# Kernel optimization log

Measured on AMD Instinct MI355X. Metric: run time of the kernel, lower is better.

## Reference

```python
import jax, jax.numpy as jnp
import numpy as np

BN_EPS = 1e-5

def setup_inputs() -> dict:
    key = jax.random.key(0)
    ks = jax.random.split(key, 4)
    B, C, H, W = 8, 64, 128, 128
    return {
        "x": jax.random.normal(ks[0], (B, C, H, W), jnp.float32),
        "w_reduce": jax.random.normal(ks[1], (C, C), jnp.float32) * 0.05,
        "b_reduce": jnp.zeros((C,), jnp.float32),
        "bn_gamma": jnp.ones((C,), jnp.float32),
        "bn_beta": jnp.zeros((C,), jnp.float32),
        "w_span": jax.random.normal(ks[2], (9, C), jnp.float32) * 0.05,
        "b_span": jnp.zeros((9,), jnp.float32),
        "w_conv2": jax.random.normal(ks[3], (C, C, 3, 3), jnp.float32) * 0.02,
        "b_conv2": jnp.zeros((C,), jnp.float32),
    }


def _involution(x, w_reduce, b_reduce, bn_gamma, bn_beta, w_span, b_span):
    # Involution2d: in_ch == out_ch so initial_mapping is Identity; groups=1, reduce_ratio=1, stride=1.
    B, C, H, W = x.shape
    # unfold 3x3, pad 1 -> patches [B, C, 9, H, W] (torch unfold ordering: C major, then kh, kw)
    xp = jnp.pad(x, ((0, 0), (0, 0), (1, 1), (1, 1)))
    patches = jnp.stack(
        [xp[:, :, i:i + H, j:j + W] for i in range(3) for j in range(3)], axis=2
    )  # [B, C, 9, H, W]
    # kernel generation: 1x1 conv -> BatchNorm2d (batch stats) -> ReLU -> 1x1 conv
    r = jnp.einsum('oc,bchw->bohw', w_reduce, x) + b_reduce[None, :, None, None]
    mu = r.mean(axis=(0, 2, 3), keepdims=True)
    var = r.var(axis=(0, 2, 3), keepdims=True)
    rn = (r - mu) * jax.lax.rsqrt(var + BN_EPS)
    rn = jax.nn.relu(rn * bn_gamma[None, :, None, None] + bn_beta[None, :, None, None])
    kern = jnp.einsum('kc,bchw->bkhw', w_span, rn) + b_span[None, :, None, None]  # [B, 9, H, W]
    # per-pixel dynamic kernel applied to patches, summed over kernel axis
    return jnp.einsum('bkhw,bckhw->bchw', kern, patches)


def reference(x, w_reduce, b_reduce, bn_gamma, bn_beta, w_span, b_span, w_conv2, b_conv2):
    z = jax.nn.softplus(_involution(x, w_reduce, b_reduce, bn_gamma, bn_beta, w_span, b_span))
    y = jax.lax.conv_general_dilated(z, w_conv2, window_strides=(1, 1), padding=((1, 1), (1, 1)))
    y = y + b_conv2[None, :, None, None]
    return jax.nn.softplus(y)
```

## Files before the change

kernel.cpp:

```cpp
#include <hip/hip_runtime.h>
#include <math.h>

#define H_ 128
#define W_ 128
#define C_ 64
#define B_ 8
#define HW 16384
#define NPIX (B_*HW)

typedef __attribute__((ext_vector_type(8))) short short8;
typedef __attribute__((ext_vector_type(4))) float f32x4;

__device__ __forceinline__ float softplus_fast(float v) {
    return fmaxf(v, 0.f) + __logf(1.f + __expf(-fabsf(v)));
}

__device__ __forceinline__ unsigned short f2bf(float f) {
    unsigned u = __builtin_bit_cast(unsigned, f);
    unsigned r = (u + 0x7fffu + ((u >> 16) & 1u)) >> 16;
    return (unsigned short)r;
}

__device__ __forceinline__ void gl_lds16(const float* g, float* l) {
    __builtin_amdgcn_global_load_lds(
        (const __attribute__((address_space(1))) void*)g,
        (__attribute__((address_space(3))) void*)l, 16, 0, 0);
}

__global__ __launch_bounds__(256) void k0_wtr(const float* __restrict__ w2,
                                              const float* __restrict__ wr,
                                              const float* __restrict__ wspan,
                                              unsigned short* __restrict__ wtr,
                                              unsigned short* __restrict__ wtr1,
                                              unsigned short* __restrict__ wtr2,
                                              float* __restrict__ stats)
{
    int t = blockIdx.x * 256 + threadIdx.x;
    if (t < 256) stats[t] = 0.f;
    if (t < 512) {
        int lane = t & 63, f = t >> 6;
        int mt = f >> 1, kh = f & 1;
        int o  = mt * 16 + (lane & 15);
        int c0 = kh * 32 + ((lane >> 4) << 3);
        uint4 pk;
        unsigned short* pv = (unsigned short*)&pk;
#pragma unroll
        for (int e = 0; e < 8; ++e)
            pv[e] = f2bf(wr[o * C_ + c0 + e]);
        *(uint4*)&wtr1[(size_t)t * 8] = pk;
    } else if (t < 640) {
        int tt = t - 512;
        int lane = tt & 63, kh = tt >> 6;
        int o  = lane & 15;
        int c0 = (kh << 5) + ((lane >> 4) << 3);
        uint4 pk;
        unsigned short* pv = (unsigned short*)&pk;
#pragma unroll
        for (int e = 0; e < 8; ++e)
            pv[e] = (o < 9) ? f2bf(wspan[o * C_ + c0 + e]) : (unsigned short)0;
        *(uint4*)&wtr2[(size_t)tt * 8] = pk;
    }
    if (t >= 4 * 18 * 64) return;
    int lane = t & 63;
    int f    = (t >> 6) % 18;
    int wv   = t / (18 * 64);
    int koff = f >> 1, ch = f & 1;
    int o = wv * 16 + (lane & 15);
    int cb = ch * 32 + ((lane >> 4) << 3);
    uint4 pk;
    unsigned short* pv = (unsigned short*)&pk;
#pragma unroll
    for (int e = 0; e < 8; ++e)
        pv[e] = f2bf(w2[(size_t)o * 576 + (size_t)(cb + e) * 9 + koff]);
    *(uint4*)&wtr[(size_t)t * 8] = pk;
}

__global__ __launch_bounds__(256) void k1_mfma(
    const float* __restrict__ x, const unsigned short* __restrict__ wtr1,
    const float* __restrict__ br, unsigned short* __restrict__ rb,
    float* __restrict__ stats)
{
    __shared__ unsigned short xb[256 * 64];
    __shared__ float brs[C_];
    __shared__ float ls[128];
    int tid = threadIdx.x;
    int blk = blockIdx.x;
    int pid0 = blk << 8;
    int b    = pid0 >> 14;
    int rem0 = pid0 & (HW - 1);
    const float* xbase = x + (((size_t)b * C_) << 14) + rem0;

    if (tid < C_) brs[tid] = br[tid];
    if (tid < 128) ls[tid] = 0.f;

    int p = tid;
#pragma unroll
    for (int m = 0; m < 8; ++m) {
        float tmp[8];
#pragma unroll
        for (int e = 0; e < 8; ++e)
            tmp[e] = xbase[((size_t)(m * 8 + e) << 14) + p];
        unsigned pk[4];
#pragma unroll
        for (int e = 0; e < 4; ++e)
            pk[e] = (unsigned)f2bf(tmp[2 * e]) | ((unsigned)f2bf(tmp[2 * e + 1]) << 16);
        *(uint4*)&xb[(p << 6) + ((m ^ (p & 7)) << 3)] = *(uint4*)pk;
    }

    int wid = tid >> 6, lane = tid & 63;
    int nl  = lane & 15;
    int kg  = lane >> 4;

    short8 af[8];
    const short8* wp = (const short8*)wtr1;
#pragma unroll
    for (int f = 0; f < 8; ++f) af[f] = wp[f * 64 + lane];

    f32x4 acc[4][4];
#pragma unroll
    for (int mt = 0; mt < 4; ++mt)
#pragma unroll
        for (int nt = 0; nt < 4; ++nt) acc[mt][nt] = (f32x4){0.f, 0.f, 0.f, 0.f};

    __syncthreads();

    int nbase = wid << 6;
#pragma unroll
    for (int nt = 0; nt < 4; ++nt) {
        int pp = nbase + (nt << 4) + nl;
#pragma unroll
        for (int kh = 0; kh < 2; ++kh) {
            int m = kh * 4 + kg;
            short8 bf = *(const short8*)&xb[(pp << 6) + ((m ^ (pp & 7)) << 3)];
#pragma unroll
            for (int mt = 0; mt < 4; ++mt)
                acc[mt][nt] = __builtin_amdgcn_mfma_f32_16x16x32_bf16(
                    af[mt * 2 + kh], bf, acc[mt][nt], 0, 0, 0);
        }
    }

    __syncthreads();

    float s_[16], q_[16];
#pragma unroll
    for (int i = 0; i < 16; ++i) { s_[i] = 0.f; q_[i] = 0.f; }

#pragma unroll
    for (int mt = 0; mt < 4; ++mt) {
        int c = (mt << 4) + (kg << 2);
        float b0 = brs[c], b1 = brs[c + 1], b2v = brs[c + 2], b3 = brs[c + 3];
        int chunk = c >> 3;
#pragma unroll
        for (int nt = 0; nt < 4; ++nt) {
            int pp = nbase + (nt << 4) + nl;
            f32x4 a = acc[mt][nt];
            float v0 = a[0] + b0, v1 = a[1] + b1, v2 = a[2] + b2v, v3 = a[3] + b3;
            s_[mt * 4 + 0] += v0; q_[mt * 4 + 0] += v0 * v0;
            s_[mt * 4 + 1] += v1; q_[mt * 4 + 1] += v1 * v1;
            s_[mt * 4 + 2] += v2; q_[mt * 4 + 2] += v2 * v2;
            s_[mt * 4 + 3] += v3; q_[mt * 4 + 3] += v3 * v3;
            unsigned lo = (unsigned)f2bf(v0) | ((unsigned)f2bf(v1) << 16);
            unsigned hi = (unsigned)f2bf(v2) | ((unsigned)f2bf(v3) << 16);
            unsigned* dst = (unsigned*)&xb[(pp << 6) + ((chunk ^ (pp & 7)) << 3) + ((kg & 1) << 2)];
            dst[0] = lo;
            dst[1] = hi;
        }
    }

#pragma unroll
    for (int i = 0; i < 16; ++i) {
#pragma unroll
        for (int m = 1; m <= 8; m <<= 1) {
            s_[i] += __shfl_xor(s_[i], m, 64);
            q_[i] += __shfl_xor(q_[i], m, 64);
        }
    }
    if (nl == 0) {
#pragma unroll
        for (int i = 0; i < 16; ++i) {
            int c = ((i >> 2) << 4) + (kg << 2) + (i & 3);
            atomicAdd(&ls[c], s_[i]);
            atomicAdd(&ls[64 + c], q_[i]);
        }
    }
    __syncthreads();
    if (tid < 128) atomicAdd(&stats[tid], ls[tid]);

    uint4* rp = (uint4*)(rb + ((size_t)(pid0 + p) << 6));
#pragma unroll
    for (int m = 0; m < 8; ++m)
        rp[m] = *(const uint4*)&xb[(p << 6) + ((m ^ (p & 7)) << 3)];
}

__global__ __launch_bounds__(256) void k34_fused(
    const float* __restrict__ x, const unsigned short* __restrict__ rb,
    const float* __restrict__ stats, const float* __restrict__ gamma,
    const float* __restrict__ beta, const unsigned short* __restrict__ wtr2,
    const float* __restrict__ bspan, const unsigned short* __restrict__ wtr,
    const float* __restrict__ b2, float* __restrict__ out)
{
    __shared__ float xh0[8 * 20 * 24], xh1[8 * 20 * 24];
    __shared__ unsigned short zt[324 * 64];
    __shared__ float a_s[C_], c_s[C_];

    int tid = threadIdx.x;
    if (tid < C_) {
        float inv_n = 1.f / (float)NPIX;
        float mu  = stats[tid] * inv_n;
        float var = stats[C_ + tid] * inv_n - mu * mu;
        float is  = rsqrtf(var + 1e-5f);
        float a   = gamma[tid] * is;
        a_s[tid] = a;
        c_s[tid] = beta[tid] - mu * a;
    }

    int blk = blockIdx.x;
    int b = blk >> 6, t = blk & 63;
    int h0 = (t >> 3) << 4, w0 = (t & 7) << 4;
    const float* xb_ = x + (((size_t)b * C_) << 14);
    const float* zgz = stats + 128;

    int goff[4];
#pragma unroll
    for (int k = 0; k < 4; ++k) {
        int item = (k << 8) + tid;
        int c    = item / 120;
        int rem  = item - c * 120;
        int row  = rem / 6;
        int ii   = rem - row * 6;
        int gh   = h0 + row - 2;
        int gw   = w0 - 4 + (ii << 2);
        bool ok = (item < 960) && ((unsigned)gh < 128u) && ((unsigned)gw < 128u);
        goff[k] = ok ? ((c << 14) + (gh << 7) + gw) : -1;
    }

    auto stage = [&](int g, float* buf) {
#pragma unroll
        for (int k = 0; k < 4; ++k) {
            if (k < 3 || tid < 192) {
                int item = (k << 8) + tid;
                const float* src = (goff[k] >= 0) ? (xb_ + (g << 17) + goff[k]) : zgz;
                gl_lds16(src, buf + (item << 2));
            }
        }
    };

    int lane = tid & 63;
    int w_  = tid >> 6;
    int nl  = lane & 15;
    int kg  = lane >> 4;
    short8 af0 = ((const short8*)wtr2)[lane];
    short8 af1 = ((const short8*)wtr2)[64 + lane];

    stage(0, xh0);
    __syncthreads();
    stage(1, xh1);

    float aa[2][8], cc[2][8];
#pragma unroll
    for (int kh = 0; kh < 2; ++kh) {
        int cb = (kh << 5) + (kg << 3);
#pragma unroll
        for (int e = 0; e < 8; ++e) { aa[kh][e] = a_s[cb + e]; cc[kh][e] = c_s[cb + e]; }
    }

    float* kl = (float*)zt;
#pragma unroll
    for (int nt = 0; nt < 6; ++nt) {
        int col = (nt << 2) + w_;
        if (col < 21) {
            int hp = (col << 4) + nl;
            int py = hp / 18, px = hp - py * 18;
            int gh = h0 + py - 1, gw = w0 + px - 1;
            int ghc = min(max(gh, 0), 127), gwc = min(max(gw, 0), 127);
            int pid2 = (b << 14) + (ghc << 7) + gwc;
            f32x4 acc9 = (f32x4){0.f, 0.f, 0.f, 0.f};
#pragma unroll
            for (int kh = 0; kh < 2; ++kh) {
                uint4 rv = *(const uint4*)(rb + ((size_t)pid2 << 6) + (kh << 5) + (kg << 3));
                const unsigned* ru = (const unsigned*)&rv;
                unsigned po[4];
#pragma unroll
                for (int e2 = 0; e2 < 4; ++e2) {
                    float lo = __builtin_bit_cast(float, ru[e2] << 16);
                    float hi = __builtin_bit_cast(float, ru[e2] & 0xffff0000u);
                    float r0 = fmaxf(aa[kh][2 * e2]     * lo + cc[kh][2 * e2],     0.f);
                    float r1 = fmaxf(aa[kh][2 * e2 + 1] * hi + cc[kh][2 * e2 + 1], 0.f);
                    po[e2] = (unsigned)f2bf(r0) | ((unsigned)f2bf(r1) << 16);
                }
                short8 bfrag = __builtin_bit_cast(short8, *(uint4*)po);
                acc9 = __builtin_amdgcn_mfma_f32_16x16x32_bf16(
                    kh ? af1 : af0, bfrag, acc9, 0, 0, 0);
            }
#pragma unroll
            for (int e = 0; e < 4; ++e) {
                int rr = (kg << 2) + e;
                if (rr < 9) kl[hp * 9 + rr] = acc9[e];
            }
        }
    }
    __syncthreads();

    float kern0[9], kern1[9];
#pragma unroll
    for (int k = 0; k < 9; ++k) kern0[k] = kl[tid * 9 + k] + bspan[k];
    bool has2 = tid < 68;
    if (has2) {
#pragma unroll
        for (int k = 0; k < 9; ++k) kern1[k] = kl[(256 + tid) * 9 + k] + bspan[k];
    }
    __syncthreads();

    int py0 = tid / 18, px0 = tid - py0 * 18;
    bool ib0 = ((unsigned)(h0 + py0 - 1) < 128u) && ((unsigned)(w0 + px0 - 1) < 128u);
    int hp1 = 256 + tid;
    int py1 = hp1 / 18, px1 = hp1 - py1 * 18;
    bool ib1 = has2 && ((unsigned)(h0 + py1 - 1) < 128u) && ((unsigned)(w0 + px1 - 1) < 128u);

    short8 wf[18];
    const short8* wp = (const short8*)wtr;
#pragma unroll
    for (int f = 0; f < 18; ++f)
        wf[f] = wp[(size_t)(w_ * 18 + f) * 64 + lane];

#pragma unroll 1
    for (int g = 0; g < 8; ++g) {
        if (g >= 1 && g < 7) stage(g + 1, (g & 1) ? xh0 : xh1);
        const float* xf = (g & 1) ? xh1 : xh0;

        unsigned pk[4];
        if (ib0) {
#pragma unroll
            for (int cp = 0; cp < 4; ++cp) {
                const float* p0 = xf + (cp * 2) * 480 + py0 * 24 + px0 + 2;
                const float* p1 = p0 + 480;
                float acc0 = 0.f, acc1 = 0.f;
#pragma unroll
                for (int i = 0; i < 3; ++i)
#pragma unroll
                    for (int j = 0; j < 3; ++j) {
                        float kv = kern0[i * 3 + j];
                        acc0 += kv * p0[i * 24 + j];
                        acc1 += kv * p1[i * 24 + j];
                    }
                pk[cp] = (unsigned)f2bf(softplus_fast(acc0))
                       | ((unsigned)f2bf(softplus_fast(acc1)) << 16);
            }
        } else {
#pragma unroll
            for (int cp = 0; cp < 4; ++cp) pk[cp] = 0u;
        }
        *(uint4*)&zt[(tid << 6) + ((g ^ (tid & 7)) << 3)] = *(uint4*)pk;

        if (has2) {
            if (ib1) {
#pragma unroll
                for (int cp = 0; cp < 4; ++cp) {
                    const float* p0 = xf + (cp * 2) * 480 + py1 * 24 + px1 + 2;
                    const float* p1 = p0 + 480;
                    float acc0 = 0.f, acc1 = 0.f;
#pragma unroll
                    for (int i = 0; i < 3; ++i)
#pragma unroll
                        for (int j = 0; j < 3; ++j) {
                            float kv = kern1[i * 3 + j];
                            acc0 += kv * p0[i * 24 + j];
                            acc1 += kv * p1[i * 24 + j];
                        }
                    pk[cp] = (unsigned)f2bf(softplus_fast(acc0))
                           | ((unsigned)f2bf(softplus_fast(acc1)) << 16);
                }
            } else {
#pragma unroll
                for (int cp = 0; cp < 4; ++cp) pk[cp] = 0u;
            }
            *(uint4*)&zt[(hp1 << 6) + ((g ^ (hp1 & 7)) << 3)] = *(uint4*)pk;
        }
        if (g < 7) __syncthreads();
    }
    __syncthreads();

    f32x4 acc[16];
#pragma unroll
    for (int nt = 0; nt < 16; ++nt) acc[nt] = (f32x4){0.f, 0.f, 0.f, 0.f};

#pragma unroll
    for (int y = 0; y < 18; ++y) {
        short8 bf[6];
#pragma unroll
        for (int j = 0; j < 3; ++j)
#pragma unroll
            for (int ch = 0; ch < 2; ++ch) {
                int p  = y * 18 + j + nl;
                int cg = ch * 4 + kg;
                bf[j * 2 + ch] = *(const short8*)&zt[(p << 6) + ((cg ^ (p & 7)) << 3)];
            }
#pragma unroll
        for (int i = 0; i < 3; ++i) {
            int nt = y - i;
            if (nt >= 0 && nt < 16) {
#pragma unroll
                for (int j = 0; j < 3; ++j)
#pragma unroll
                    for (int ch = 0; ch < 2; ++ch)
                        acc[nt] = __builtin_amdgcn_mfma_f32_16x16x32_bf16(
                            wf[(i * 3 + j) * 2 + ch], bf[j * 2 + ch], acc[nt], 0, 0, 0);
            }
        }
    }

    float bias[4];
#pragma unroll
    for (int r = 0; r < 4; ++r) bias[r] = b2[(w_ << 4) + (kg << 2) + r];

    size_t ob = ((size_t)b) << 20;
#pragma unroll
    for (int nt = 0; nt < 16; ++nt) {
        int h = h0 + nt;
#pragma unroll
        for (int r = 0; r < 4; ++r) {
            int o = (w_ << 4) + (kg << 2) + r;
            float v = acc[nt][r] + bias[r];
            out[ob + ((size_t)o << 14) + (h << 7) + w0 + nl] = softplus_fast(v);
        }
    }
}

extern "C" void kernel_launch(void* const* d_in, const int* in_sizes, int n_in,
                              void* d_out, int out_size, void* d_ws, size_t ws_size,
                              hipStream_t stream)
{
    const float* x   = (const float*)d_in[0];
    const float* wr  = (const float*)d_in[1];
    const float* br  = (const float*)d_in[2];
    const float* gam = (const float*)d_in[3];
    const float* bet = (const float*)d_in[4];
    const float* wsp = (const float*)d_in[5];
    const float* bsp = (const float*)d_in[6];
    const float* w2  = (const float*)d_in[7];
    const float* b2  = (const float*)d_in[8];
    float* out = (float*)d_out;

    unsigned short* rb   = (unsigned short*)d_ws;
    unsigned short* wtr  = rb + (size_t)NPIX * C_;
    unsigned short* wtr1 = wtr + 4608 * 8;
    unsigned short* wtr2 = wtr1 + 512 * 8;
    float* stats = (float*)(wtr2 + 128 * 8);

    k0_wtr<<<18, 256, 0, stream>>>(w2, wr, wsp, wtr, wtr1, wtr2, stats);
    k1_mfma<<<NPIX / 256, 256, 0, stream>>>(x, wtr1, br, rb, stats);
    k34_fused<<<NPIX / 256, 256, 0, stream>>>(x, rb, stats, gam, bet, wtr2, bsp,
                                              wtr, b2, out);
}
```

Baseline: 81.15 us.

## Split conv2 into two channel halves to halve LDS z-tile and weight registers

The z tile in shared memory is halved to hold 32 channels at a time. The involution and softplus stage fills the first 32 channels, then the conv MFMA pass runs over them with only 9 weight fragments in registers, and the process repeats for the second half. This cuts LDS footprint and VGPR pressure, which could allow more blocks per CU. The cost is an extra barrier, a serialization point between the two halves, and a second pass over the z tile for the conv.

```diff
diff --git a/kernel.cpp b/kernel.cpp
--- a/kernel.cpp
+++ b/kernel.cpp
@@ -200,7 +200,7 @@
     const float* __restrict__ b2, float* __restrict__ out)
 {
     __shared__ float xh0[8 * 20 * 24], xh1[8 * 20 * 24];
-    __shared__ unsigned short zt[324 * 64];
+    __shared__ unsigned short zt[324 * 32];
     __shared__ float a_s[C_], c_s[C_];
 
     int tid = threadIdx.x;
@@ -317,17 +317,9 @@
     int py1 = hp1 / 18, px1 = hp1 - py1 * 18;
     bool ib1 = has2 && ((unsigned)(h0 + py1 - 1) < 128u) && ((unsigned)(w0 + px1 - 1) < 128u);
 
-    short8 wf[18];
-    const short8* wp = (const short8*)wtr;
-#pragma unroll
-    for (int f = 0; f < 18; ++f)
-        wf[f] = wp[(size_t)(w_ * 18 + f) * 64 + lane];
-
-#pragma unroll 1
-    for (int g = 0; g < 8; ++g) {
-        if (g >= 1 && g < 7) stage(g + 1, (g & 1) ? xh0 : xh1);
+    auto computeZ = [&](int g) {
         const float* xf = (g & 1) ? xh1 : xh0;
-
+        int cgz = g & 3;
         unsigned pk[4];
         if (ib0) {
 #pragma unroll
@@ -350,7 +342,7 @@
 #pragma unroll
             for (int cp = 0; cp < 4; ++cp) pk[cp] = 0u;
         }
-        *(uint4*)&zt[(tid << 6) + ((g ^ (tid & 7)) << 3)] = *(uint4*)pk;
+        *(uint4*)&zt[(tid << 5) + ((cgz ^ ((tid >> 1) & 3)) << 3)] = *(uint4*)pk;
 
         if (has2) {
             if (ib1) {
@@ -374,40 +366,57 @@
 #pragma unroll
                 for (int cp = 0; cp < 4; ++cp) pk[cp] = 0u;
             }
-            *(uint4*)&zt[(hp1 << 6) + ((g ^ (hp1 & 7)) << 3)] = *(uint4*)pk;
-        }
-        if (g < 7) __syncthreads();
-    }
-    __syncthreads();
+            *(uint4*)&zt[(hp1 << 5) + ((cgz ^ ((hp1 >> 1) & 3)) << 3)] = *(uint4*)pk;
+        }
+    };
 
     f32x4 acc[16];
 #pragma unroll
     for (int nt = 0; nt < 16; ++nt) acc[nt] = (f32x4){0.f, 0.f, 0.f, 0.f};
 
-#pragma unroll
-    for (int y = 0; y < 18; ++y) {
-        short8 bf[6];
-#pragma unroll
-        for (int j = 0; j < 3; ++j)
-#pragma unroll
-            for (int ch = 0; ch < 2; ++ch) {
-                int p  = y * 18 + j + nl;
-                int cg = ch * 4 + kg;
-                bf[j * 2 + ch] = *(const short8*)&zt[(p << 6) + ((cg ^ (p & 7)) << 3)];
-            }
-#pragma unroll
-        for (int i = 0; i < 3; ++i) {
-            int nt = y - i;
-            if (nt >= 0 && nt < 16) {
-#pragma unroll
-                for (int j = 0; j < 3; ++j)
-#pragma unroll
-                    for (int ch = 0; ch < 2; ++ch)
+    const short8* wp = (const short8*)wtr;
+    auto convHalf = [&](int half) {
+        short8 wfh[9];
+#pragma unroll
+        for (int f9 = 0; f9 < 9; ++f9)
+            wfh[f9] = wp[(size_t)(w_ * 18 + f9 * 2 + half) * 64 + lane];
+#pragma unroll
+        for (int y = 0; y < 18; ++y) {
+            short8 bf[3];
+#pragma unroll
+            for (int j = 0; j < 3; ++j) {
+                int p = y * 18 + j + nl;
+                bf[j] = *(const short8*)&zt[(p << 5) + ((kg ^ ((p >> 1) & 3)) << 3)];
+            }
+#pragma unroll
+            for (int i = 0; i < 3; ++i) {
+                int nt = y - i;
+                if (nt >= 0 && nt < 16) {
+#pragma unroll
+                    for (int j = 0; j < 3; ++j)
                         acc[nt] = __builtin_amdgcn_mfma_f32_16x16x32_bf16(
-                            wf[(i * 3 + j) * 2 + ch], bf[j * 2 + ch], acc[nt], 0, 0, 0);
-            }
-        }
-    }
+                            wfh[i * 3 + j], bf[j], acc[nt], 0, 0, 0);
+                }
+            }
+        }
+    };
+
+#pragma unroll 1
+    for (int g = 0; g < 4; ++g) {
+        if (g >= 1) stage(g + 1, (g & 1) ? xh0 : xh1);
+        computeZ(g);
+        __syncthreads();
+    }
+    convHalf(0);
+    __syncthreads();
+
+#pragma unroll 1
+    for (int g = 4; g < 8; ++g) {
+        if (g < 7) stage(g + 1, (g & 1) ? xh0 : xh1);
+        computeZ(g);
+        __syncthreads();
+    }
+    convHalf(1);
 
     float bias[4];
 #pragma unroll
```

Result: slower. 99.27 us (+22.3%).

## Use 512 threads in fused involution-conv kernel, splitting conv rows across waves

Applied to the files above, without the earlier changes.

Doubles the block size of the fused kernel to 512 threads. Each thread now handles at most one halo pixel in the involution stage instead of two. The 3x3 conv MFMA stage is split across 8 waves as 4 output-channel groups times 2 row halves. Conv weights are loaded per channel half (9 fragments instead of 18) to cut register pressure. The aim is more waves in flight and shorter per-wave serial work, at the cost of duplicated halo-row reads in the conv stage and a higher thread count per block.

```diff
diff --git a/kernel.cpp b/kernel.cpp
--- a/kernel.cpp
+++ b/kernel.cpp
@@ -192,7 +192,7 @@
         rp[m] = *(const uint4*)&xb[(p << 6) + ((m ^ (p & 7)) << 3)];
 }
 
-__global__ __launch_bounds__(256) void k34_fused(
+__global__ __launch_bounds__(512, 4) void k34_fused(
     const float* __restrict__ x, const unsigned short* __restrict__ rb,
     const float* __restrict__ stats, const float* __restrict__ gamma,
     const float* __restrict__ beta, const unsigned short* __restrict__ wtr2,
@@ -220,10 +220,10 @@
     const float* xb_ = x + (((size_t)b * C_) << 14);
     const float* zgz = stats + 128;
 
-    int goff[4];
-#pragma unroll
-    for (int k = 0; k < 4; ++k) {
-        int item = (k << 8) + tid;
+    int goff[2];
+#pragma unroll
+    for (int k = 0; k < 2; ++k) {
+        int item = (k << 9) + tid;
         int c    = item / 120;
         int rem  = item - c * 120;
         int row  = rem / 6;
@@ -236,9 +236,9 @@
 
     auto stage = [&](int g, float* buf) {
 #pragma unroll
-        for (int k = 0; k < 4; ++k) {
-            if (k < 3 || tid < 192) {
-                int item = (k << 8) + tid;
+        for (int k = 0; k < 2; ++k) {
+            if (k == 0 || tid < 448) {
+                int item = (k << 9) + tid;
                 const float* src = (goff[k] >= 0) ? (xb_ + (g << 17) + goff[k]) : zgz;
                 gl_lds16(src, buf + (item << 2));
             }
@@ -266,8 +266,8 @@
 
     float* kl = (float*)zt;
 #pragma unroll
-    for (int nt = 0; nt < 6; ++nt) {
-        int col = (nt << 2) + w_;
+    for (int i3 = 0; i3 < 3; ++i3) {
+        int col = w_ * 3 + i3;
         if (col < 21) {
             int hp = (col << 4) + nl;
             int py = hp / 18, px = hp - py * 18;
@@ -301,69 +301,34 @@
     }
     __syncthreads();
 
-    float kern0[9], kern1[9];
-#pragma unroll
-    for (int k = 0; k < 9; ++k) kern0[k] = kl[tid * 9 + k] + bspan[k];
-    bool has2 = tid < 68;
-    if (has2) {
-#pragma unroll
-        for (int k = 0; k < 9; ++k) kern1[k] = kl[(256 + tid) * 9 + k] + bspan[k];
+    bool hasPix = tid < 324;
+    float kern0[9];
+    if (hasPix) {
+#pragma unroll
+        for (int k = 0; k < 9; ++k) kern0[k] = kl[tid * 9 + k] + bspan[k];
     }
     __syncthreads();
 
     int py0 = tid / 18, px0 = tid - py0 * 18;
-    bool ib0 = ((unsigned)(h0 + py0 - 1) < 128u) && ((unsigned)(w0 + px0 - 1) < 128u);
-    int hp1 = 256 + tid;
-    int py1 = hp1 / 18, px1 = hp1 - py1 * 18;
-    bool ib1 = has2 && ((unsigned)(h0 + py1 - 1) < 128u) && ((unsigned)(w0 + px1 - 1) < 128u);
-
-    short8 wf[18];
-    const short8* wp = (const short8*)wtr;
-#pragma unroll
-    for (int f = 0; f < 18; ++f)
-        wf[f] = wp[(size_t)(w_ * 18 + f) * 64 + lane];
+    bool ib0 = hasPix && ((unsigned)(h0 + py0 - 1) < 128u) && ((unsigned)(w0 + px0 - 1) < 128u);
 
 #pragma unroll 1
     for (int g = 0; g < 8; ++g) {
         if (g >= 1 && g < 7) stage(g + 1, (g & 1) ? xh0 : xh1);
         const float* xf = (g & 1) ? xh1 : xh0;
-
-        unsigned pk[4];
-        if (ib0) {
-#pragma unroll
-            for (int cp = 0; cp < 4; ++cp) {
-                const float* p0 = xf + (cp * 2) * 480 + py0 * 24 + px0 + 2;
-                const float* p1 = p0 + 480;
-                float acc0 = 0.f, acc1 = 0.f;
-#pragma unroll
-                for (int i = 0; i < 3; ++i)
-#pragma unroll
-                    for (int j = 0; j < 3; ++j) {
-                        float kv = kern0[i * 3 + j];
-                        acc0 += kv * p0[i * 24 + j];
-                        acc1 += kv * p1[i * 24 + j];
-                    }
-                pk[cp] = (unsigned)f2bf(softplus_fast(acc0))
-                       | ((unsigned)f2bf(softplus_fast(acc1)) << 16);
-            }
-        } else {
-#pragma unroll
-            for (int cp = 0; cp < 4; ++cp) pk[cp] = 0u;
-        }
-        *(uint4*)&zt[(tid << 6) + ((g ^ (tid & 7)) << 3)] = *(uint4*)pk;
-
-        if (has2) {
-            if (ib1) {
+        if (hasPix) {
+            unsigned pk[4];
+            if (ib0) {
 #pragma unroll
                 for (int cp = 0; cp < 4; ++cp) {
-                    const float* p0 = xf + (cp * 2) * 480 + py1 * 24 + px1 + 2;
+                    const float* p0 = xf + (cp * 2) * 480 + py0 * 24 + px0 + 2;
                     const float* p1 = p0 + 480;
                     float acc0 = 0.f, acc1 = 0.f;
 #pragma unroll
                     for (int i = 0; i < 3; ++i)
 #pragma unroll
                         for (int j = 0; j < 3; ++j) {
-                            float kv = kern1[i * 3 + j];
+                            float kv = kern0[i * 3 + j];
                             acc0 += kv * p0[i * 24 + j];
                             acc1 += kv * p1[i * 24 + j];
                         }
@@ -374,52 +339,58 @@
 #pragma unroll
                 for (int cp = 0; cp < 4; ++cp) pk[cp] = 0u;
             }
-            *(uint4*)&zt[(hp1 << 6) + ((g ^ (hp1 & 7)) << 3)] = *(uint4*)pk;
-        }
-        if (g < 7) __syncthreads();
-    }
-    __syncthreads();
-
-    f32x4 acc[16];
-#pragma unroll
-    for (int nt = 0; nt < 16; ++nt) acc[nt] = (f32x4){0.f, 0.f, 0.f, 0.f};
-
-#pragma unroll
-    for (int y = 0; y < 18; ++y) {
-        short8 bf[6];
-#pragma unroll
-        for (int j = 0; j < 3; ++j)
-#pragma unroll
-            for (int ch = 0; ch < 2; ++ch) {
-                int p  = y * 18 + j + nl;
-                int cg = ch * 4 + kg;
-                bf[j * 2 + ch] = *(const short8*)&zt[(p << 6) + ((cg ^ (p & 7)) << 3)];
-            }
-#pragma unroll
-        for (int i = 0; i < 3; ++i) {
-            int nt = y - i;
-            if (nt >= 0 && nt < 16) {
-#pragma unroll
-                for (int j = 0; j < 3; ++j)
-#pragma unroll
-                    for (int ch = 0; ch < 2; ++ch)
+            *(uint4*)&zt[(tid << 6) + ((g ^ (tid & 7)) << 3)] = *(uint4*)pk;
+        }
+        __syncthreads();
+    }
+
+    int og = w_ & 3, yh = w_ >> 2;
+    int ybase = yh << 3;
+    f32x4 acc[8];
+#pragma unroll
+    for (int nt = 0; nt < 8; ++nt) acc[nt] = (f32x4){0.f, 0.f, 0.f, 0.f};
+
+    const short8* wp = (const short8*)wtr;
+#pragma unroll
+    for (int kh = 0; kh < 2; ++kh) {
+        short8 wfh[9];
+#pragma unroll
+        for (int f9 = 0; f9 < 9; ++f9)
+            wfh[f9] = wp[(size_t)(og * 18 + f9 * 2 + kh) * 64 + lane];
+        int cg = kh * 4 + kg;
+#pragma unroll
+        for (int yy = 0; yy < 10; ++yy) {
+            int y = ybase + yy;
+            short8 bf[3];
+#pragma unroll
+            for (int j = 0; j < 3; ++j) {
+                int p = y * 18 + j + nl;
+                bf[j] = *(const short8*)&zt[(p << 6) + ((cg ^ (p & 7)) << 3)];
+            }
+#pragma unroll
+            for (int i = 0; i < 3; ++i) {
+                int nt = yy - i;
+                if (nt >= 0 && nt < 8) {
+#pragma unroll
+                    for (int j = 0; j < 3; ++j)
                         acc[nt] = __builtin_amdgcn_mfma_f32_16x16x32_bf16(
-                            wf[(i * 3 + j) * 2 + ch], bf[j * 2 + ch], acc[nt], 0, 0, 0);
+                            wfh[i * 3 + j], bf[j], acc[nt], 0, 0, 0);
+                }
             }
         }
     }
 
     float bias[4];
 #pragma unroll
-    for (int r = 0; r < 4; ++r) bias[r] = b2[(w_ << 4) + (kg << 2) + r];
+    for (int r = 0; r < 4; ++r) bias[r] = b2[(og << 4) + (kg << 2) + r];
 
     size_t ob = ((size_t)b) << 20;
 #pragma unroll
-    for (int nt = 0; nt < 16; ++nt) {
-        int h = h0 + nt;
+    for (int nt = 0; nt < 8; ++nt) {
+        int h = h0 + ybase + nt;
 #pragma unroll
         for (int r = 0; r < 4; ++r) {
-            int o = (w_ << 4) + (kg << 2) + r;
+            int o = (og << 4) + (kg << 2) + r;
             float v = acc[nt][r] + bias[r];
             out[ob + ((size_t)o << 14) + (h << 7) + w0 + nl] = softplus_fast(v);
         }
@@ -449,6 +420,6 @@
 
     k0_wtr<<<18, 256, 0, stream>>>(w2, wr, wsp, wtr, wtr1, wtr2, stats);
     k1_mfma<<<NPIX / 256, 256, 0, stream>>>(x, wtr1, br, rb, stats);
-    k34_fused<<<NPIX / 256, 256, 0, stream>>>(x, rb, stats, gam, bet, wtr2, bsp,
+    k34_fused<<<NPIX / 256, 512, 0, stream>>>(x, rb, stats, gam, bet, wtr2, bsp,
                                               wtr, b2, out);
 }
```

Measured after the change: 76.90 us. -5.2%, faster.
